# Kernel optimization log

Hardware: AMD Instinct MI355X
Metric: run time of the kernel (lower is better)

The kernel has to match this reference:

```python
import jax, jax.numpy as jnp
import numpy as np

X = 2048      # hidden units per layer
Z = 4         # number of hidden layers
IN = 512      # input_dim
OUT = 256     # output_dim
B = 64        # batch
T = 128       # time steps
KEEP = 0.7    # Bernoulli keep prob y
RES = [0, 0, 1, 2]  # residual_in (first two unused by the branch structure)
NFUN = 5      # number of candidate transfer functions


def setup_inputs() -> dict:
    key = jax.random.key(0)
    ks = jax.random.split(key, 12)
    f32 = jnp.float32
    x = jax.random.normal(ks[0], (B, T, IN), f32)
    W_in = jax.random.normal(ks[1], (X, IN), f32) * jax.random.bernoulli(ks[2], KEEP, (X, IN)).astype(f32)
    b_in = jax.random.normal(ks[3], (X,), f32)
    W_h = jax.random.normal(ks[4], (Z, X, 2 * X), f32)
    # lateral inhibition block: hidden layer 1, second-half columns, zero diagonal
    lat = jax.random.normal(ks[5], (X, X), f32) * (1.0 - jnp.eye(X, dtype=f32))
    W_h = W_h.at[1, :, X:].set(lat)
    W_h = W_h * jax.random.bernoulli(ks[6], KEEP, (Z, X, 2 * X)).astype(f32)
    b_h = jax.random.normal(ks[7], (Z, X), f32)
    W_out = jax.random.normal(ks[8], (OUT, X), f32) * jax.random.bernoulli(ks[9], KEEP, (OUT, X)).astype(f32)
    b_out = jax.random.normal(ks[10], (OUT,), f32)
    act_ids = jax.random.randint(ks[11], (Z + 1, X), 0, NFUN)
    out_act_ids = jax.random.randint(jax.random.fold_in(key, 99), (OUT,), 0, NFUN)
    return dict(x=x, W_in=W_in, b_in=b_in, W_h=W_h, b_h=b_h,
                W_out=W_out, b_out=b_out, act_ids=act_ids, out_act_ids=out_act_ids)


def _rand_act(h, ids):
    # per-column random nonlinearity: ids [D] in {relu, sigmoid, tanh, leaky_relu(0.1), selu}
    stk = jnp.stack([
        jax.nn.relu(h),
        jax.nn.sigmoid(h),
        jnp.tanh(h),
        jnp.where(h >= 0, h, 0.1 * h),
        jax.nn.selu(h),
    ], axis=0)  # [5, B, D]
    oh = jax.nn.one_hot(ids, NFUN, dtype=h.dtype)  # [D, 5]
    return jnp.einsum('fbd,df->bd', stk, oh)


def _l2norm(v, eps=1e-12):
    # torch F.normalize along dim=1
    return v / jnp.maximum(jnp.linalg.norm(v, axis=1, keepdims=True), eps)


def reference(x, W_in, b_in, W_h, b_h, W_out, b_out, act_ids, out_act_ids):
    batch = x.shape[0]

    def step(carry, xt):
        bp, li = carry  # backprojection state, lateral inhibition state
        h0 = _rand_act(xt @ W_in.T + b_in, act_ids[0])
        h1 = _rand_act(jnp.concatenate([h0, bp], axis=-1) @ W_h[0].T + b_h[0], act_ids[1])
        h2 = _rand_act(jnp.concatenate([h1, li], axis=-1) @ W_h[1].T + b_h[1], act_ids[2])
        li_new = _l2norm(h2)
        outs = [h0, h1, h2]
        for i in range(2, Z):
            hin = jnp.concatenate([outs[i], outs[RES[i]]], axis=-1)
            outs.append(_rand_act(hin @ W_h[i].T + b_h[i], act_ids[i + 1]))
        bp_new = _l2norm(outs[-1])
        yt = _rand_act(outs[-1] @ W_out.T + b_out, out_act_ids)
        return (bp_new, li_new), yt

    init = (jnp.zeros((batch, X), x.dtype), jnp.zeros((batch, X), x.dtype))
    _, ys = jax.lax.scan(step, init, jnp.swapaxes(x, 0, 1))  # scan over time
    return jnp.swapaxes(ys, 0, 1)  # [B, T, OUT]
```

## Files before the change

kernel.cpp:

```cpp
#include <hip/hip_runtime.h>
#include <stdint.h>


typedef __bf16 bf16;
typedef __attribute__((ext_vector_type(8))) __bf16 bf16x8;
typedef __attribute__((ext_vector_type(4))) float f32x4;

#define BATCH 64
#define TSTEPS 128
#define INDIM 512
#define XDIM 2048
#define OUTDIM 256
#define SLOTE ((size_t)BATCH * XDIM)

__device__ __forceinline__ float apply_act(float h, int id) {
  switch (id) {
    case 0: return fmaxf(h, 0.0f);
    case 1: return 1.0f / (1.0f + __expf(-h));
    case 2: return tanhf(h);
    case 3: return h >= 0.0f ? h : 0.1f * h;
    default: {
      const float sc = 1.0507009873554805f;
      const float al = 1.6732632423543772f;
      return h > 0.0f ? sc * h : sc * al * (__expf(h) - 1.0f);
    }
  }
}

template <bool SCALE_A2, bool EMIT_SS>
__global__ __launch_bounds__(512, 2) void step_gemm8(
    const bf16* __restrict__ A1, const bf16* __restrict__ A2,
    const bf16* __restrict__ W, const float* __restrict__ bias,
    const int* __restrict__ acts, const float* __restrict__ ss_in,
    float* __restrict__ ss_out, bf16* __restrict__ outb) {
  const int tid = threadIdx.x;
  const int lane = tid & 63;
  const int w = tid >> 6;
  const int l15 = lane & 15;
  const int kb8 = (lane >> 4) * 8;
  const int nblk = blockIdx.x * 16;
  const int mrow = blockIdx.y * 32;

  const bf16* As = (w >= 4) ? A2 : A1;
  const int koff = (w & 3) * 512;
  const int wk = w * 512;

  const bf16* ap0 = As + (size_t)(mrow + l15) * 2048 + koff + kb8;
  const bf16* ap1 = ap0 + 16 * 2048;
  const bf16* bpw = W + (size_t)(nblk + l15) * 4096 + wk + kb8;

  f32x4 acc0 = {0.f, 0.f, 0.f, 0.f};
  f32x4 acc1 = {0.f, 0.f, 0.f, 0.f};
#pragma unroll
  for (int k = 0; k < 512; k += 32) {
    bf16x8 a0 = *(const bf16x8*)(ap0 + k);
    bf16x8 a1 = *(const bf16x8*)(ap1 + k);
    bf16x8 b  = *(const bf16x8*)(bpw + k);
    acc0 = __builtin_amdgcn_mfma_f32_16x16x32_bf16(a0, b, acc0, 0, 0, 0);
    acc1 = __builtin_amdgcn_mfma_f32_16x16x32_bf16(a1, b, acc1, 0, 0, 0);
  }

  __shared__ float red[8][32][17];
  const int q4 = lane >> 4;
#pragma unroll
  for (int r = 0; r < 4; r++) red[w][q4 * 4 + r][l15] = acc0[r];
#pragma unroll
  for (int r = 0; r < 4; r++) red[w][16 + q4 * 4 + r][l15] = acc1[r];
  __syncthreads();

  if (tid < 256) {
    const int row = tid >> 3;
    const int c0 = (tid & 7) * 2;
    const int rg = mrow + row;

    float scale = 1.0f;
    if (SCALE_A2) scale = 1.0f / fmaxf(sqrtf(ss_in[rg]), 1e-12f);

    float v[2];
#pragma unroll
    for (int j = 0; j < 2; j++) {
      int c = c0 + j;
      float lo = red[0][row][c] + red[1][row][c] + red[2][row][c] + red[3][row][c];
      float hi = red[4][row][c] + red[5][row][c] + red[6][row][c] + red[7][row][c];
      float pre = (SCALE_A2 ? (lo + scale * hi) : (lo + hi)) + bias[nblk + c];
      v[j] = apply_act(pre, acts[nblk + c]);
    }
    if (EMIT_SS) {
      float ss = v[0] * v[0] + v[1] * v[1];
      ss += __shfl_xor(ss, 1);
      ss += __shfl_xor(ss, 2);
      ss += __shfl_xor(ss, 4);
      if ((tid & 7) == 0) atomicAdd(ss_out + rg, ss);
    }
    union { bf16 b2[2]; uint32_t u; } pk;
    pk.b2[0] = (bf16)v[0];
    pk.b2[1] = (bf16)v[1];
    *(uint32_t*)(outb + (size_t)rg * XDIM + nblk + c0) = pk.u;
  }
}

__global__ __launch_bounds__(256) void h0_gemm(
    const bf16* __restrict__ A, const bf16* __restrict__ W,
    const float* __restrict__ bias, const int* __restrict__ acts,
    bf16* __restrict__ outp) {
  const int tid = threadIdx.x;
  const int lane = tid & 63;
  const int wv = tid >> 6;
  const int wm = (wv & 1) * 32;
  const int wn = (wv >> 1) * 64;
  const int nblk = blockIdx.x * 128;
  const int mblk = blockIdx.y * 64;
  const int l15 = lane & 15;
  const int kb8 = (lane >> 4) * 8;

  f32x4 acc[2][4];
  const f32x4 zero = {0.f, 0.f, 0.f, 0.f};
#pragma unroll
  for (int i = 0; i < 2; i++)
#pragma unroll
    for (int j = 0; j < 4; j++) acc[i][j] = zero;

  for (int kt = 0; kt < INDIM; kt += 32) {
    bf16x8 a[2], b[4];
#pragma unroll
    for (int mt = 0; mt < 2; mt++) {
      int m = mblk + wm + mt * 16 + l15;
      a[mt] = *(const bf16x8*)(A + (size_t)m * INDIM + kt + kb8);
    }
#pragma unroll
    for (int nt = 0; nt < 4; nt++) {
      int n = nblk + wn + nt * 16 + l15;
      b[nt] = *(const bf16x8*)(W + (size_t)n * INDIM + kt + kb8);
    }
#pragma unroll
    for (int mt = 0; mt < 2; mt++)
#pragma unroll
      for (int nt = 0; nt < 4; nt++)
        acc[mt][nt] = __builtin_amdgcn_mfma_f32_16x16x32_bf16(a[mt], b[nt], acc[mt][nt], 0, 0, 0);
  }

#pragma unroll
  for (int mt = 0; mt < 2; mt++) {
#pragma unroll
    for (int nt = 0; nt < 4; nt++) {
      int n = nblk + wn + nt * 16 + l15;
      float bv = bias[n];
      int aid = acts[n];
#pragma unroll
      for (int rr = 0; rr < 4; rr++) {
        int m = wm + mt * 16 + (lane >> 4) * 4 + rr;
        float v = apply_act(acc[mt][nt][rr] + bv, aid);
        int rowg = mblk + m;
        int bb = rowg >> 7;
        int tt = rowg & 127;
        outp[((size_t)tt * BATCH + bb) * XDIM + n] = (bf16)v;
      }
    }
  }
}

__global__ __launch_bounds__(256) void ybat_gemm(
    const bf16* __restrict__ extra, const bf16* __restrict__ h0,
    const bf16* __restrict__ Wout, const float* __restrict__ bout,
    const int* __restrict__ oact, float* __restrict__ out) {
  const int t = blockIdx.y;
  const int s = t + 1;
  const bf16* A = (s < 2) ? (extra + (size_t)s * SLOTE)
                          : (h0 + (size_t)(s - 2) * SLOTE);
  const int tid = threadIdx.x;
  const int lane = tid & 63;
  const int wv = tid >> 6;
  const int wm = (wv & 1) * 32;
  const int wn = (wv >> 1) * 64;
  const int nblk = blockIdx.x * 128;
  const int l15 = lane & 15;
  const int kb8 = (lane >> 4) * 8;

  f32x4 acc[2][4];
  const f32x4 zero = {0.f, 0.f, 0.f, 0.f};
#pragma unroll
  for (int i = 0; i < 2; i++)
#pragma unroll
    for (int j = 0; j < 4; j++) acc[i][j] = zero;

  for (int kt = 0; kt < XDIM; kt += 32) {
    bf16x8 a[2], b[4];
#pragma unroll
    for (int mt = 0; mt < 2; mt++) {
      int m = wm + mt * 16 + l15;
      a[mt] = *(const bf16x8*)(A + (size_t)m * XDIM + kt + kb8);
    }
#pragma unroll
    for (int nt = 0; nt < 4; nt++) {
      int n = nblk + wn + nt * 16 + l15;
      b[nt] = *(const bf16x8*)(Wout + (size_t)n * XDIM + kt + kb8);
    }
#pragma unroll
    for (int mt = 0; mt < 2; mt++)
#pragma unroll
      for (int nt = 0; nt < 4; nt++)
        acc[mt][nt] = __builtin_amdgcn_mfma_f32_16x16x32_bf16(a[mt], b[nt], acc[mt][nt], 0, 0, 0);
  }

#pragma unroll
  for (int mt = 0; mt < 2; mt++) {
#pragma unroll
    for (int nt = 0; nt < 4; nt++) {
      int n = nblk + wn + nt * 16 + l15;
      float bv = bout[n];
      int aid = oact[n];
#pragma unroll
      for (int rr = 0; rr < 4; rr++) {
        int b = wm + mt * 16 + (lane >> 4) * 4 + rr;
        float v = apply_act(acc[mt][nt][rr] + bv, aid);
        out[((size_t)b * TSTEPS + t) * OUTDIM + n] = v;
      }
    }
  }
}

__global__ __launch_bounds__(256) void cvt_bf16(
    const float* __restrict__ in, bf16* __restrict__ out, int n4) {
  int i = blockIdx.x * 256 + threadIdx.x;
  if (i < n4) {
    float4 v = ((const float4*)in)[i];
    union { bf16 b[4]; unsigned long long u; } pk;
    pk.b[0] = (bf16)v.x;
    pk.b[1] = (bf16)v.y;
    pk.b[2] = (bf16)v.z;
    pk.b[3] = (bf16)v.w;
    ((unsigned long long*)out)[i] = pk.u;
  }
}

__global__ __launch_bounds__(256) void zero32(uint32_t* __restrict__ p, int n) {
  int i = blockIdx.x * 256 + threadIdx.x;
  if (i < n) p[i] = 0u;
}

extern "C" void kernel_launch(void* const* d_in, const int* in_sizes, int n_in,
                              void* d_out, int out_size, void* d_ws, size_t ws_size,
                              hipStream_t stream) {
  const float* x     = (const float*)d_in[0];
  const float* W_in  = (const float*)d_in[1];
  const float* b_in  = (const float*)d_in[2];
  const float* W_h   = (const float*)d_in[3];
  const float* b_h   = (const float*)d_in[4];
  const float* W_out = (const float*)d_in[5];
  const float* b_out = (const float*)d_in[6];
  const int* act_ids = (const int*)d_in[7];
  const int* out_act = (const int*)d_in[8];
  float* out = (float*)d_out;

  char* w = (char*)d_ws;
  bf16* xbf   = (bf16*)w; w += (size_t)BATCH * TSTEPS * INDIM * 2;
  bf16* winb  = (bf16*)w; w += (size_t)XDIM * INDIM * 2;
  bf16* whb   = (bf16*)w; w += (size_t)4 * XDIM * (2 * XDIM) * 2;
  bf16* woutb = (bf16*)w; w += (size_t)OUTDIM * XDIM * 2;
  bf16* h0    = (bf16*)w; w += (size_t)TSTEPS * SLOTE * 2;
  bf16* h1    = (bf16*)w; w += SLOTE * 2;
  bf16* h3    = (bf16*)w; w += SLOTE * 2;
  char* zstart = w;
  bf16* extra = (bf16*)w; w += 2 * SLOTE * 2;
  bf16* h2a   = (bf16*)w; w += SLOTE * 2;
  bf16* h2b   = (bf16*)w; w += SLOTE * 2;
  float* ss_li = (float*)w; w += (size_t)(TSTEPS + 1) * BATCH * 4;
  float* ss_bp = (float*)w; w += (size_t)(TSTEPS + 1) * BATCH * 4;
  int zero_u32 = (int)((w - zstart) / 4);

  cvt_bf16<<<4096, 256, 0, stream>>>(x, xbf, (BATCH * TSTEPS * INDIM) / 4);
  cvt_bf16<<<1024, 256, 0, stream>>>(W_in, winb, (XDIM * INDIM) / 4);
  cvt_bf16<<<32768, 256, 0, stream>>>(W_h, whb, (4 * XDIM * 2 * XDIM) / 4);
  cvt_bf16<<<512, 256, 0, stream>>>(W_out, woutb, (OUTDIM * XDIM) / 4);
  zero32<<<(zero_u32 + 255) / 256, 256, 0, stream>>>((uint32_t*)zstart, zero_u32);
  h0_gemm<<<dim3(16, 128), 256, 0, stream>>>(xbf, winb, b_in, act_ids, h0);

  auto slotp = [&](int s) -> bf16* {
    return (s < 2) ? (extra + (size_t)s * SLOTE) : (h0 + (size_t)(s - 2) * SLOTE);
  };

  const size_t wstr = (size_t)XDIM * 2 * XDIM;
  for (int t = 0; t < TSTEPS; t++) {
    bf16* h2n = (t & 1) ? h2b : h2a;
    bf16* h2o = (t & 1) ? h2a : h2b;

    step_gemm8<true, false><<<dim3(128, 2), 512, 0, stream>>>(
        h0 + (size_t)t * SLOTE, slotp(t), whb, b_h, act_ids + XDIM,
        ss_bp + t * BATCH, nullptr, h1);
    step_gemm8<true, true><<<dim3(128, 2), 512, 0, stream>>>(
        h1, h2o, whb + wstr, b_h + XDIM, act_ids + 2 * XDIM,
        ss_li + t * BATCH, ss_li + (t + 1) * BATCH, h2n);
    step_gemm8<false, false><<<dim3(128, 2), 512, 0, stream>>>(
        h2n, h1, whb + 2 * wstr, b_h + 2 * XDIM, act_ids + 3 * XDIM,
        nullptr, nullptr, h3);
    step_gemm8<false, true><<<dim3(128, 2), 512, 0, stream>>>(
        h3, h2n, whb + 3 * wstr, b_h + 3 * XDIM, act_ids + 4 * XDIM,
        nullptr, ss_bp + (t + 1) * BATCH, slotp(t + 1));
  }

  ybat_gemm<<<dim3(2, TSTEPS), 256, 0, stream>>>(
      extra, h0, woutb, b_out, out_act, out);
}
```

Baseline: 8.867 ms.

## Replace per-step kernel launches with persistent cooperative kernel and grid barriers

Replaces the 512 small per-timestep GEMM launches with one cooperative persistent kernel of 256 workgroups that loops over time and layers. Layers are separated by a hierarchical atomic grid barrier. Cross-workgroup activations are read and written with agent-scope relaxed atomics so stale caches are not read. The tile is remapped from 32 rows by 16 columns to 16 rows by 32 columns, so each A fragment feeds two B fragments. This targets launch overhead and inter-kernel gaps, at the cost of barrier spin latency and uncached coherent loads.

```diff
diff --git a/kernel.cpp b/kernel.cpp
--- a/kernel.cpp
+++ b/kernel.cpp
@@ -11,6 +11,7 @@
 #define INDIM 512
 #define XDIM 2048
 #define OUTDIM 256
+#define NWG 256
 #define SLOTE ((size_t)BATCH * XDIM)
 
 __device__ __forceinline__ float apply_act(float h, int id) {
@@ -27,54 +28,107 @@
   }
 }
 
-template <bool SCALE_A2, bool EMIT_SS>
-__global__ __launch_bounds__(512, 2) void step_gemm8(
+__device__ __forceinline__ bf16x8 load_n(const bf16* p) {
+  return *(const bf16x8*)p;
+}
+__device__ __forceinline__ bf16x8 load_c(const bf16* p) {
+  union { unsigned long long q[2]; bf16x8 v; } u;
+  u.q[0] = __hip_atomic_load((const unsigned long long*)p, __ATOMIC_RELAXED,
+                             __HIP_MEMORY_SCOPE_AGENT);
+  u.q[1] = __hip_atomic_load((const unsigned long long*)p + 1, __ATOMIC_RELAXED,
+                             __HIP_MEMORY_SCOPE_AGENT);
+  return u.v;
+}
+
+__device__ __forceinline__ void gbar(uint32_t* bar, int wg, uint32_t bt) {
+  asm volatile("s_waitcnt vmcnt(0)" ::: "memory");
+  __syncthreads();
+  if (threadIdx.x == 0) {
+    const int g = wg >> 5;
+    uint32_t* grp = bar + g * 32;
+    uint32_t* root = bar + 8 * 32;
+    uint32_t* eps = bar + 9 * 32 + g * 32;
+    uint32_t prev = __hip_atomic_fetch_add(grp, 1u, __ATOMIC_RELAXED,
+                                           __HIP_MEMORY_SCOPE_AGENT);
+    if (prev == 32u * bt - 1u) {
+      uint32_t pr = __hip_atomic_fetch_add(root, 1u, __ATOMIC_RELAXED,
+                                           __HIP_MEMORY_SCOPE_AGENT);
+      if (pr == 8u * bt - 1u) {
+        for (int i = 0; i < 8; i++)
+          __hip_atomic_store(bar + 9 * 32 + i * 32, bt, __ATOMIC_RELAXED,
+                             __HIP_MEMORY_SCOPE_AGENT);
+        goto done;
+      }
+    }
+    while (__hip_atomic_load(eps, __ATOMIC_RELAXED, __HIP_MEMORY_SCOPE_AGENT) < bt)
+      __builtin_amdgcn_s_sleep(2);
+  done:;
+  }
+  __syncthreads();
+}
+
+template <bool ALL_COH, bool SCALE_A2, bool EMIT_SS>
+__device__ __forceinline__ void phase(
+    int nblk, int mrow,
     const bf16* __restrict__ A1, const bf16* __restrict__ A2,
     const bf16* __restrict__ W, const float* __restrict__ bias,
     const int* __restrict__ acts, const float* __restrict__ ss_in,
-    float* __restrict__ ss_out, bf16* __restrict__ outb) {
+    float* __restrict__ ss_out, bf16* __restrict__ outb,
+    float red[8][16][33]) {
   const int tid = threadIdx.x;
   const int lane = tid & 63;
   const int w = tid >> 6;
   const int l15 = lane & 15;
   const int kb8 = (lane >> 4) * 8;
-  const int nblk = blockIdx.x * 16;
-  const int mrow = blockIdx.y * 32;
 
   const bf16* As = (w >= 4) ? A2 : A1;
   const int koff = (w & 3) * 512;
   const int wk = w * 512;
 
-  const bf16* ap0 = As + (size_t)(mrow + l15) * 2048 + koff + kb8;
-  const bf16* ap1 = ap0 + 16 * 2048;
-  const bf16* bpw = W + (size_t)(nblk + l15) * 4096 + wk + kb8;
+  const bf16* ap = As + (size_t)(mrow + l15) * 2048 + koff + kb8;
+  const bf16* bp0 = W + (size_t)(nblk + l15) * 4096 + wk + kb8;
+  const bf16* bp1 = bp0 + (size_t)16 * 4096;
 
   f32x4 acc0 = {0.f, 0.f, 0.f, 0.f};
   f32x4 acc1 = {0.f, 0.f, 0.f, 0.f};
-#pragma unroll
-  for (int k = 0; k < 512; k += 32) {
-    bf16x8 a0 = *(const bf16x8*)(ap0 + k);
-    bf16x8 a1 = *(const bf16x8*)(ap1 + k);
-    bf16x8 b  = *(const bf16x8*)(bpw + k);
-    acc0 = __builtin_amdgcn_mfma_f32_16x16x32_bf16(a0, b, acc0, 0, 0, 0);
-    acc1 = __builtin_amdgcn_mfma_f32_16x16x32_bf16(a1, b, acc1, 0, 0, 0);
-  }
-
-  __shared__ float red[8][32][17];
+  if (ALL_COH || w >= 4) {
+#pragma unroll
+    for (int k = 0; k < 512; k += 32) {
+      bf16x8 a = load_c(ap + k);
+      bf16x8 b0 = load_n(bp0 + k);
+      bf16x8 b1 = load_n(bp1 + k);
+      acc0 = __builtin_amdgcn_mfma_f32_16x16x32_bf16(a, b0, acc0, 0, 0, 0);
+      acc1 = __builtin_amdgcn_mfma_f32_16x16x32_bf16(a, b1, acc1, 0, 0, 0);
+    }
+  } else {
+#pragma unroll
+    for (int k = 0; k < 512; k += 32) {
+      bf16x8 a = load_n(ap + k);
+      bf16x8 b0 = load_n(bp0 + k);
+      bf16x8 b1 = load_n(bp1 + k);
+      acc0 = __builtin_amdgcn_mfma_f32_16x16x32_bf16(a, b0, acc0, 0, 0, 0);
+      acc1 = __builtin_amdgcn_mfma_f32_16x16x32_bf16(a, b1, acc1, 0, 0, 0);
+    }
+  }
+
   const int q4 = lane >> 4;
 #pragma unroll
   for (int r = 0; r < 4; r++) red[w][q4 * 4 + r][l15] = acc0[r];
 #pragma unroll
-  for (int r = 0; r < 4; r++) red[w][16 + q4 * 4 + r][l15] = acc1[r];
+  for (int r = 0; r < 4; r++) red[w][q4 * 4 + r][16 + l15] = acc1[r];
   __syncthreads();
 
   if (tid < 256) {
-    const int row = tid >> 3;
-    const int c0 = (tid & 7) * 2;
+    const int row = tid >> 4;
+    const int c0 = (tid & 15) * 2;
     const int rg = mrow + row;
 
     float scale = 1.0f;
-    if (SCALE_A2) scale = 1.0f / fmaxf(sqrtf(ss_in[rg]), 1e-12f);
+    if (SCALE_A2) {
+      float ssv = __hip_atomic_load(ss_in + rg, __ATOMIC_RELAXED,
+                                    __HIP_MEMORY_SCOPE_AGENT);
+      scale = 1.0f / fmaxf(sqrtf(ssv), 1e-12f);
+    }
 
     float v[2];
 #pragma unroll
@@ -90,12 +144,61 @@
       ss += __shfl_xor(ss, 1);
       ss += __shfl_xor(ss, 2);
       ss += __shfl_xor(ss, 4);
-      if ((tid & 7) == 0) atomicAdd(ss_out + rg, ss);
+      ss += __shfl_xor(ss, 8);
+      if ((tid & 15) == 0) atomicAdd(ss_out + rg, ss);
     }
     union { bf16 b2[2]; uint32_t u; } pk;
     pk.b2[0] = (bf16)v[0];
     pk.b2[1] = (bf16)v[1];
-    *(uint32_t*)(outb + (size_t)rg * XDIM + nblk + c0) = pk.u;
+    __hip_atomic_store((uint32_t*)(outb + (size_t)rg * 2048 + nblk + c0), pk.u,
+                       __ATOMIC_RELAXED, __HIP_MEMORY_SCOPE_AGENT);
+  }
+}
+
+struct Params {
+  const bf16* h0;
+  bf16* h0m;
+  const bf16* whb;
+  const float* b_h;
+  const int* act_ids;
+  bf16 *h1, *h2a, *h2b, *h3, *extra;
+  float *ss_li, *ss_bp;
+  uint32_t* bar;
+};
+
+__global__ __launch_bounds__(512, 2) void bnn_persistent(Params p) {
+  __shared__ float red[8][16][33];
+  const int wg = blockIdx.x;
+  const int nblk = (wg & 63) * 32;
+  const int mrow = (wg >> 6) * 16;
+  const size_t wstr = (size_t)XDIM * 2 * XDIM;
+  uint32_t bt = 0;
+
+  for (int t = 0; t < TSTEPS; t++) {
+    const bf16* h0t = p.h0 + (size_t)t * SLOTE;
+    const bf16* slotA = (t < 2) ? (p.extra + (size_t)t * SLOTE)
+                                : (p.h0 + (size_t)(t - 2) * SLOTE);
+    bf16* slotD = (t + 1 < 2) ? (p.extra + (size_t)(t + 1) * SLOTE)
+                              : (p.h0m + (size_t)(t - 1) * SLOTE);
+    bf16* h2n = (t & 1) ? p.h2b : p.h2a;
+    bf16* h2o = (t & 1) ? p.h2a : p.h2b;
+
+    phase<false, true, false>(nblk, mrow, h0t, slotA, p.whb, p.b_h,
+                              p.act_ids + XDIM, p.ss_bp + t * BATCH, nullptr,
+                              p.h1, red);
+    gbar(p.bar, wg, ++bt);
+    phase<true, true, true>(nblk, mrow, p.h1, h2o, p.whb + wstr, p.b_h + XDIM,
+                            p.act_ids + 2 * XDIM, p.ss_li + t * BATCH,
+                            p.ss_li + (t + 1) * BATCH, h2n, red);
+    gbar(p.bar, wg, ++bt);
+    phase<true, false, false>(nblk, mrow, h2n, p.h1, p.whb + 2 * wstr,
+                              p.b_h + 2 * XDIM, p.act_ids + 3 * XDIM, nullptr,
+                              nullptr, p.h3, red);
+    gbar(p.bar, wg, ++bt);
+    phase<true, false, true>(nblk, mrow, p.h3, h2n, p.whb + 3 * wstr,
+                             p.b_h + 3 * XDIM, p.act_ids + 4 * XDIM, nullptr,
+                             p.ss_bp + (t + 1) * BATCH, slotD, red);
+    gbar(p.bar, wg, ++bt);
   }
 }
 
@@ -266,6 +369,7 @@
   bf16* h2b   = (bf16*)w; w += SLOTE * 2;
   float* ss_li = (float*)w; w += (size_t)(TSTEPS + 1) * BATCH * 4;
   float* ss_bp = (float*)w; w += (size_t)(TSTEPS + 1) * BATCH * 4;
+  uint32_t* bar = (uint32_t*)w; w += 17 * 32 * 4;
   int zero_u32 = (int)((w - zstart) / 4);
 
   cvt_bf16<<<4096, 256, 0, stream>>>(x, xbf, (BATCH * TSTEPS * INDIM) / 4);
@@ -275,28 +379,14 @@
   zero32<<<(zero_u32 + 255) / 256, 256, 0, stream>>>((uint32_t*)zstart, zero_u32);
   h0_gemm<<<dim3(16, 128), 256, 0, stream>>>(xbf, winb, b_in, act_ids, h0);
 
-  auto slotp = [&](int s) -> bf16* {
-    return (s < 2) ? (extra + (size_t)s * SLOTE) : (h0 + (size_t)(s - 2) * SLOTE);
-  };
-
-  const size_t wstr = (size_t)XDIM * 2 * XDIM;
-  for (int t = 0; t < TSTEPS; t++) {
-    bf16* h2n = (t & 1) ? h2b : h2a;
-    bf16* h2o = (t & 1) ? h2a : h2b;
-
-    step_gemm8<true, false><<<dim3(128, 2), 512, 0, stream>>>(
-        h0 + (size_t)t * SLOTE, slotp(t), whb, b_h, act_ids + XDIM,
-        ss_bp + t * BATCH, nullptr, h1);
-    step_gemm8<true, true><<<dim3(128, 2), 512, 0, stream>>>(
-        h1, h2o, whb + wstr, b_h + XDIM, act_ids + 2 * XDIM,
-        ss_li + t * BATCH, ss_li + (t + 1) * BATCH, h2n);
-    step_gemm8<false, false><<<dim3(128, 2), 512, 0, stream>>>(
-        h2n, h1, whb + 2 * wstr, b_h + 2 * XDIM, act_ids + 3 * XDIM,
-        nullptr, nullptr, h3);
-    step_gemm8<false, true><<<dim3(128, 2), 512, 0, stream>>>(
-        h3, h2n, whb + 3 * wstr, b_h + 3 * XDIM, act_ids + 4 * XDIM,
-        nullptr, ss_bp + (t + 1) * BATCH, slotp(t + 1));
-  }
+  Params P;
+  P.h0 = h0; P.h0m = h0; P.whb = whb; P.b_h = b_h; P.act_ids = act_ids;
+  P.h1 = h1; P.h2a = h2a; P.h2b = h2b; P.h3 = h3; P.extra = extra;
+  P.ss_li = ss_li; P.ss_bp = ss_bp; P.bar = bar;
+
+  void* kargs[] = {&P};
+  hipLaunchCooperativeKernel((const void*)bnn_persistent, dim3(NWG), dim3(512),
+                             kargs, 0, stream);
 
   ybat_gemm<<<dim3(2, TSTEPS), 256, 0, stream>>>(
       extra, h0, woutb, b_out, out_act, out);
```

Measured after the change: 10.47 ms. 18.1% more time.
